# Performance work log

Measured on AMD Instinct MI355X. Metric: run time of the kernel, lower is better.

## Reference

```python
import jax, jax.numpy as jnp
import numpy as np

N, E, B, IN = 20000, 320000, 64, 192


def setup_inputs() -> dict:
    key = jax.random.key(0)
    ks = iter(jax.random.split(key, 80))
    d = {}
    d["x"] = jax.random.normal(next(ks), (N, IN), jnp.float32)
    d["edge_index"] = jax.random.randint(next(ks), (2, E), 0, N - 1)  # +1 shift stays < N
    d["edge_attr"] = jax.random.normal(next(ks), (E,), jnp.float32)
    d["batch"] = jnp.sort(jax.random.randint(next(ks), (N,), 0, B))

    def lin(i, o):
        w = jax.random.normal(next(ks), (i, o), jnp.float32) * (1.0 / i ** 0.5)
        return w, jnp.zeros((o,), jnp.float32)

    dims = [(IN, 4, 64), (256, 4, 64), (256, 6, 32)]  # (in_ch, heads, out_ch) per conv
    for l, (ic, h, c) in enumerate(dims, 1):
        hc = h * c
        d[f"Wq{l}"], d[f"bq{l}"] = lin(ic, hc)
        d[f"Wk{l}"], d[f"bk{l}"] = lin(ic, hc)
        d[f"Wv{l}"], d[f"bv{l}"] = lin(ic, hc)
        d[f"We{l}"] = jax.random.normal(next(ks), (1, hc), jnp.float32)  # lin_edge, no bias
        d[f"Ws{l}"], d[f"bs{l}"] = lin(ic, hc)  # root/skip weight
    d["g1"] = jnp.ones((256,), jnp.float32); d["be1"] = jnp.zeros((256,), jnp.float32)
    d["g2"] = jnp.ones((256,), jnp.float32); d["be2"] = jnp.zeros((256,), jnp.float32)
    d["fc1_w"], d["fc1_b"] = lin(192, 32)
    d["fc2_w"], d["fc2_b"] = lin(32, 2)
    return d


def seg_softmax(s, seg, n):
    # per-destination-node softmax over edges, [E, H]
    m = jax.ops.segment_max(s, seg, num_segments=n)
    m = jnp.where(jnp.isfinite(m), m, 0.0)
    ex = jnp.exp(s - m[seg])
    den = jax.ops.segment_sum(ex, seg, num_segments=n)
    return ex / (den[seg] + 1e-16)


def tconv(x, src, dst, e, Wq, bq, Wk, bk, Wv, bv, We, Ws, bs, h, c):
    # PyG TransformerConv (concat=True, root_weight=True, beta=False, eval -> no dropout)
    n = x.shape[0]
    q = (x @ Wq + bq).reshape(n, h, c)
    k = (x @ Wk + bk).reshape(n, h, c)
    v = (x @ Wv + bv).reshape(n, h, c)
    ee = (e @ We).reshape(-1, h, c)           # [E, h, c] edge embedding
    kj = k[src] + ee                           # gather keys along edges
    scores = jnp.einsum('ehc,ehc->eh', q[dst], kj) * (1.0 / c ** 0.5)
    alpha = seg_softmax(scores, dst, n)        # [E, h]
    msg = (v[src] + ee) * alpha[..., None]
    out = jax.ops.segment_sum(msg, dst, num_segments=n).reshape(n, h * c)
    return out + x @ Ws + bs, alpha


def ln(x, g, b):
    mu = x.mean(-1, keepdims=True)
    var = x.var(-1, keepdims=True)
    return g * (x - mu) / jnp.sqrt(var + 1e-5) + b


def _forward(x, edge_index, edge_attr, batch, Wq1, bq1, Wk1, bk1, Wv1, bv1, We1, Ws1, bs1, Wq2, bq2, Wk2, bk2, Wv2, bv2, We2, Ws2, bs2, Wq3, bq3, Wk3, bk3, Wv3, bv3, We3, Ws3, bs3, g1, be1, g2, be2, fc1_w, fc1_b, fc2_w, fc2_b):
    ei = edge_index + 1                       # replicates `edge_index += 1` in source
    src, dst = ei[0], ei[1]
    e = edge_attr[:, None]                    # edge_dim = 1
    x1, a1 = tconv(x, src, dst, e, Wq1, bq1, Wk1, bk1, Wv1, bv1, We1, Ws1, bs1, 4, 64)
    x1 = jax.nn.relu(ln(x1, g1, be1))
    x2, a2 = tconv(x1, src, dst, e, Wq2, bq2, Wk2, bk2, Wv2, bv2, We2, Ws2, bs2, 4, 64)
    x2 = jax.nn.relu(ln(x2, g2, be2))
    x3, a3 = tconv(x2, src, dst, e, Wq3, bq3, Wk3, bk3, Wv3, bv3, We3, Ws3, bs3, 6, 32)
    x3 = jax.nn.relu(x3)                      # note: norm3 exists in __init__ but is never applied
    xr = x + x3
    cnt = jax.ops.segment_sum(jnp.ones((xr.shape[0],), xr.dtype), batch, num_segments=B)
    pooled = jax.ops.segment_sum(xr, batch, num_segments=B) / jnp.maximum(cnt, 1.0)[:, None]
    h = jax.nn.relu(pooled @ fc1_w + fc1_b)
    logits = h @ fc2_w + fc2_b
    return logits, a1, a2, a3


def reference(x, edge_index, edge_attr, batch, Wq1, bq1, Wk1, bk1, Wv1, bv1, We1, Ws1, bs1, Wq2, bq2, Wk2, bk2, Wv2, bv2, We2, Ws2, bs2, Wq3, bq3, Wk3, bk3, Wv3, bv3, We3, Ws3, bs3, g1, be1, g2, be2, fc1_w, fc1_b, fc2_w, fc2_b):
    return _forward(x, edge_index, edge_attr, batch, Wq1, bq1, Wk1, bk1, Wv1, bv1, We1, Ws1, bs1, Wq2, bq2, Wk2, bk2, Wv2, bv2, We2, Ws2, bs2, Wq3, bq3, Wk3, bk3, Wv3, bv3, We3, Ws3, bs3, g1, be1, g2, be2, fc1_w, fc1_b, fc2_w, fc2_b)
```

## Files before the change

kernel.cpp:

```cpp
#include <hip/hip_runtime.h>
#include <cstdint>
#include <cstddef>

#define DEVINL __device__ __forceinline__

typedef short s16x8 __attribute__((ext_vector_type(8)));
typedef float f32x4 __attribute__((ext_vector_type(4)));
typedef unsigned short u16x4 __attribute__((ext_vector_type(4)));
typedef unsigned short u16x8 __attribute__((ext_vector_type(8)));

DEVINL unsigned short f2bf(float f) {
  unsigned u = __float_as_uint(f);
  unsigned r = (u + 0x7FFFu + ((u >> 16) & 1u)) >> 16;
  return (unsigned short)r;
}
DEVINL float bf2f(unsigned short b) { return __uint_as_float(((unsigned)b) << 16); }

__global__ __launch_bounds__(256) void fill_i32(int* __restrict__ p, int val, int n) {
  int i = blockIdx.x * 256 + threadIdx.x;
  if (i < n) p[i] = val;
}


__global__ __launch_bounds__(256) void cvt_split(const float* __restrict__ in,
                                                 unsigned short* __restrict__ hi,
                                                 unsigned short* __restrict__ lo, int n) {
  int i = blockIdx.x * 256 + threadIdx.x;
  if (i >= n) return;
  float f = in[i];
  unsigned short h = f2bf(f);
  float r = f - bf2f(h);
  hi[i] = h;
  lo[i] = f2bf(r);
}

struct CvtWArgs {
  const float* W[12];
  int K[12];
  int M[12];
};
__global__ __launch_bounds__(256) void cvt_w_all(CvtWArgs a,
                                                 unsigned short* __restrict__ Wh,
                                                 unsigned short* __restrict__ Wl) {
  int tid = blockIdx.x * 256 + threadIdx.x;
  int mat = tid >> 16;
  int off = tid & 65535;
  if (mat >= 12) return;
  int K = a.K[mat], M = a.M[mat];
  if (off >= K * M) return;
  int k = off / M, m = off - k * M;
  float f = a.W[mat][off];
  unsigned short h = f2bf(f);
  float r = f - bf2f(h);
  size_t dst = (size_t)mat * 65536 + (size_t)m * K + k;
  Wh[dst] = h;
  Wl[dst] = f2bf(r);
}

struct GemmArgs {
  const unsigned short* Wh[4];
  const unsigned short* Wl[4];
  const float* bias[4];
  float* out[4];
  int obf[4];
};

template <int KTOT>
__global__ __launch_bounds__(256, 3) void gemm4_lds(
    const unsigned short* __restrict__ Ah, const unsigned short* __restrict__ Al,
    GemmArgs args, int N, int M) {
  const int BK = 64;
  __shared__ unsigned short ash[128 * 64];
  __shared__ unsigned short asl[128 * 64];
  __shared__ unsigned short wsh[64 * 64];
  __shared__ unsigned short wsl[64 * 64];
  int tid = threadIdx.x;
  int wave = tid >> 6, lane = tid & 63;
  int lrow = lane & 15, quad = lane >> 4;
  int mt = M >> 6;
  int ntile = mt * 4;
  int id = blockIdx.x, nwg = gridDim.x;
  int q8 = nwg >> 3, r8 = nwg & 7;
  int xcd = id & 7, j8 = id >> 3;
  int wg = (xcd < r8 ? xcd * (q8 + 1) : r8 * (q8 + 1) + (xcd - r8) * q8) + j8;
  int by = wg / ntile;
  int bxx = wg - by * ntile;
  int z = bxx / mt;
  int colTile = bxx - z * mt;
  int row0 = by * 128;
  int col0 = colTile * 64;
  const unsigned short* __restrict__ Wh = args.Wh[z];
  const unsigned short* __restrict__ Wl = args.Wl[z];
  const bool full = (args.obf[z] == 0);

  int ar[4], asq[4];
  size_t agoff[4];
#pragma unroll
  for (int i = 0; i < 4; i++) {
    int c = tid + i * 256;
    ar[i] = c >> 3;
    int kq = c & 7;
    asq[i] = kq ^ (ar[i] & 7);
    int gr = row0 + ar[i]; if (gr >= N) gr = N - 1;
    agoff[i] = (size_t)gr * KTOT + kq * 8;
  }
  int wr[2], wsq[2];
  size_t wgoff[2];
#pragma unroll
  for (int i = 0; i < 2; i++) {
    int c = tid + i * 256;
    wr[i] = c >> 3;
    int kq = c & 7;
    wsq[i] = kq ^ (wr[i] & 7);
    wgoff[i] = (size_t)(col0 + wr[i]) * KTOT + kq * 8;
  }

  s16x8 pa_h[4], pa_l[4], pw_h[2], pw_l[2];
#pragma unroll
  for (int i = 0; i < 4; i++) {
    pa_h[i] = *(const s16x8*)(Ah + agoff[i]);
    pa_l[i] = *(const s16x8*)(Al + agoff[i]);
  }
#pragma unroll
  for (int i = 0; i < 2; i++) {
    pw_h[i] = *(const s16x8*)(Wh + wgoff[i]);
    if (full) pw_l[i] = *(const s16x8*)(Wl + wgoff[i]);
  }

  f32x4 acc[2][4] = {};

  for (int k0 = 0; k0 < KTOT; k0 += BK) {
    __syncthreads();
#pragma unroll
    for (int i = 0; i < 4; i++) {
      *(s16x8*)(ash + ar[i] * 64 + asq[i] * 8) = pa_h[i];
      *(s16x8*)(asl + ar[i] * 64 + asq[i] * 8) = pa_l[i];
    }
#pragma unroll
    for (int i = 0; i < 2; i++) {
      *(s16x8*)(wsh + wr[i] * 64 + wsq[i] * 8) = pw_h[i];
      if (full) *(s16x8*)(wsl + wr[i] * 64 + wsq[i] * 8) = pw_l[i];
    }
    if (k0 + BK < KTOT) {
      int kn = k0 + BK;
#pragma unroll
      for (int i = 0; i < 4; i++) {
        pa_h[i] = *(const s16x8*)(Ah + agoff[i] + kn);
        pa_l[i] = *(const s16x8*)(Al + agoff[i] + kn);
      }
#pragma unroll
      for (int i = 0; i < 2; i++) {
        pw_h[i] = *(const s16x8*)(Wh + wgoff[i] + kn);
        if (full) pw_l[i] = *(const s16x8*)(Wl + wgoff[i] + kn);
      }
    }
    __syncthreads();
#pragma unroll
    for (int kk = 0; kk < 2; kk++) {
      s16x8 fah[2], fal[2], fbh[4], fbl[4];
#pragma unroll
      for (int rf = 0; rf < 2; rf++) {
        int r = wave * 32 + rf * 16 + lrow;
        int sq = (kk * 4 + quad) ^ (lrow & 7);
        fah[rf] = *(const s16x8*)(ash + r * 64 + sq * 8);
        fal[rf] = *(const s16x8*)(asl + r * 64 + sq * 8);
      }
#pragma unroll
      for (int cf = 0; cf < 4; cf++) {
        int cc = cf * 16 + lrow;
        int sq = (kk * 4 + quad) ^ (lrow & 7);
        fbh[cf] = *(const s16x8*)(wsh + cc * 64 + sq * 8);
        if (full) fbl[cf] = *(const s16x8*)(wsl + cc * 64 + sq * 8);
      }
#pragma unroll
      for (int rf = 0; rf < 2; rf++)
#pragma unroll
        for (int cf = 0; cf < 4; cf++) {
          acc[rf][cf] = __builtin_amdgcn_mfma_f32_16x16x32_bf16(fah[rf], fbh[cf], acc[rf][cf], 0, 0, 0);
          acc[rf][cf] = __builtin_amdgcn_mfma_f32_16x16x32_bf16(fal[rf], fbh[cf], acc[rf][cf], 0, 0, 0);
          if (full)
            acc[rf][cf] = __builtin_amdgcn_mfma_f32_16x16x32_bf16(fah[rf], fbl[cf], acc[rf][cf], 0, 0, 0);
        }
    }
  }
  const float* __restrict__ bias = args.bias[z];
  int obf = args.obf[z];
  if (obf == 0) {
    float* __restrict__ C = args.out[z];
#pragma unroll
    for (int cf = 0; cf < 4; cf++) {
      int col = col0 + cf * 16 + lrow;
      float bv = bias[col];
#pragma unroll
      for (int rf = 0; rf < 2; rf++) {
        int rb = row0 + wave * 32 + rf * 16 + quad * 4;
#pragma unroll
        for (int r = 0; r < 4; r++) {
          int rr = rb + r;
          if (rr < N) C[(size_t)rr * M + col] = acc[rf][cf][r] + bv;
        }
      }
    }
  } else {
    __syncthreads();
#pragma unroll
    for (int cf = 0; cf < 4; cf++) {
      int col = cf * 16 + lrow;
      float bv = bias[col0 + col];
#pragma unroll
      for (int rf = 0; rf < 2; rf++) {
        int rl = wave * 32 + rf * 16 + quad * 4;
#pragma unroll
        for (int r = 0; r < 4; r++)
          ash[(rl + r) * 64 + col] = f2bf(acc[rf][cf][r] + bv);
      }
    }
    __syncthreads();
    unsigned short* __restrict__ C = (unsigned short*)args.out[z];
#pragma unroll
    for (int i = 0; i < 4; i++) {
      int c = tid + i * 256;
      int row = c >> 3, g8 = c & 7;
      int rr = row0 + row;
      if (rr < N)
        *(u16x8*)(C + (size_t)rr * M + col0 + g8 * 8) =
            *(const u16x8*)(ash + row * 64 + g8 * 8);
    }
  }
}


__global__ __launch_bounds__(256) void hist_dst(const int* __restrict__ dst,
                                                int* __restrict__ cnt, int E) {
  int e = blockIdx.x * 256 + threadIdx.x;
  if (e < E) atomicAdd(&cnt[dst[e] + 1], 1);
}

__global__ __launch_bounds__(1024) void scan_hist(const int* __restrict__ cnt,
                                                  int* __restrict__ start,
                                                  int* __restrict__ off, int N) {
  __shared__ int sums[1024];
  const int CH = 20;
  int t = threadIdx.x;
  int base = t * CH;
  int local[CH];
  int tot = 0;
  if (base < N) {
#pragma unroll
    for (int i = 0; i < CH; i++) { local[i] = cnt[base + i]; tot += local[i]; }
  }
  sums[t] = tot;
  __syncthreads();
  for (int d = 1; d < 1024; d <<= 1) {
    int v = (t >= d) ? sums[t - d] : 0;
    __syncthreads();
    sums[t] += v;
    __syncthreads();
  }
  if (base < N) {
    int run = (t == 0) ? 0 : sums[t - 1];
#pragma unroll
    for (int i = 0; i < CH; i++) { start[base + i] = run; off[base + i] = run; run += local[i]; }
    if (base + CH == N) start[N] = run;
  }
}

__global__ __launch_bounds__(256) void scatter_edges(
    const int* __restrict__ src, const int* __restrict__ dst,
    const float* __restrict__ ea, int* __restrict__ off,
    int2* __restrict__ se, int* __restrict__ eid_s, int E) {
  int e = blockIdx.x * 256 + threadIdx.x;
  if (e >= E) return;
  int d = dst[e] + 1;
  int pos = atomicAdd(&off[d], 1);
  se[pos] = make_int2(src[e] + 1, __float_as_int(ea[e]));
  eid_s[pos] = e;
}

template <int H, int ACT, int MODE>
__global__ __launch_bounds__(256) void attn_fused(
    const unsigned short* __restrict__ q, const unsigned short* __restrict__ kb,
    const unsigned short* __restrict__ vb, const float* __restrict__ We,
    const int* __restrict__ start, const int2* __restrict__ se,
    const int* __restrict__ eid_s,
    float* __restrict__ sc, float* __restrict__ outp,
    float* __restrict__ alpha, int Nn, float scale,
    const float* __restrict__ gam, const float* __restrict__ bet,
    unsigned short* __restrict__ hi, unsigned short* __restrict__ lo) {
  const int HC = ACT * 8;
  const int LPH2 = ACT / H;
  int w = (blockIdx.x * 256 + threadIdx.x) >> 6;
  int lane = threadIdx.x & 63;
  if (w >= Nn) return;
  int b = start[w], e = start[w + 1];
  int hlane = lane & 31, half = lane >> 5;
  bool act = hlane < ACT;
  int idx = hlane * 8;
  int head = hlane / LPH2;
  float q8[8], We8[8];
#pragma unroll
  for (int j = 0; j < 8; j++) { q8[j] = 0.f; We8[j] = 0.f; }
  if (act) {
    u16x8 qv = *(const u16x8*)(q + (size_t)w * HC + idx);
#pragma unroll
    for (int j = 0; j < 8; j++) q8[j] = bf2f(qv[j]);
    float4 w0 = *(const float4*)(We + idx);
    float4 w1 = *(const float4*)(We + idx + 4);
    We8[0] = w0.x; We8[1] = w0.y; We8[2] = w0.z; We8[3] = w0.w;
    We8[4] = w1.x; We8[5] = w1.y; We8[6] = w1.z; We8[7] = w1.w;
  }
  float qwe = 0.f;
#pragma unroll
  for (int j = 0; j < 8; j++) qwe = fmaf(q8[j], We8[j], qwe);
#pragma unroll
  for (int mm = 1; mm < LPH2; mm <<= 1) qwe += __shfl_xor(qwe, mm, 64);

  float l = 0.f, tv = 0.f;
  float accv[8] = {0.f, 0.f, 0.f, 0.f, 0.f, 0.f, 0.f, 0.f};

  auto step = [&](u16x8 kc, u16x8 vc, float eav, int pairpos) {
    bool vld = (pairpos + half) < e;
    float p = 0.f;
#pragma unroll
    for (int j = 0; j < 8; j++) p = fmaf(q8[j], bf2f(kc[j]), p);
#pragma unroll
    for (int mm = 1; mm < LPH2; mm <<= 1) p += __shfl_xor(p, mm, 64);
    float es = __expf((p + eav * qwe) * scale);
    if (!vld) es = 0.f;
    if (act && vld && (hlane % LPH2) == 0)
      sc[(size_t)(pairpos + half) * H + head] = es;
    l += es;
    tv = fmaf(es, eav, tv);
#pragma unroll
    for (int j = 0; j < 8; j++) accv[j] = fmaf(es, bf2f(vc[j]), accv[j]);
  };

  u16x8 z8 = {0, 0, 0, 0, 0, 0, 0, 0};
  u16x8 kS[4] = {z8, z8, z8, z8};
  u16x8 vS[4] = {z8, z8, z8, z8};
  float eaS[4] = {0.f, 0.f, 0.f, 0.f};

  auto preload = [&](int pairpos, int st) {
    int pp = pairpos + half;
    int pc = pp < e ? pp : (e - 1);
    int2 pr = se[pc];
    int s = pr.x;
    eaS[st] = __int_as_float(pr.y);
    if (act) {
      kS[st] = *(const u16x8*)(kb + (size_t)s * HC + idx);
      vS[st] = *(const u16x8*)(vb + (size_t)s * HC + idx);
    }
  };

#pragma unroll
  for (int j = 0; j < 4; j++) if (b + 2 * j < e) preload(b + 2 * j, j);

  for (int pos = b; pos < e; pos += 8) {
#pragma unroll
    for (int j = 0; j < 4; j++) {
      int pp = pos + 2 * j;
      if (pp < e) {
        u16x8 kc = kS[j];
        u16x8 vc = vS[j];
        float ec = eaS[j];
        if (pp + 8 < e) preload(pp + 8, j);
        step(kc, vc, ec, pp);
      }
    }
  }

  l += __shfl_xor(l, 32, 64);
  tv += __shfl_xor(tv, 32, 64);
#pragma unroll
  for (int j = 0; j < 8; j++) accv[j] += __shfl_xor(accv[j], 32, 64);

  float invl = 1.0f / (l + 1e-16f);
  if (MODE == 1) {
    if (half == 0) {
      const float* orow = outp + (size_t)w * HC + idx;
      float4 o0 = *(const float4*)orow;
      float4 o1 = *(const float4*)(orow + 4);
      float y[8] = {o0.x, o0.y, o0.z, o0.w, o1.x, o1.y, o1.z, o1.w};
#pragma unroll
      for (int j = 0; j < 8; j++) y[j] += (accv[j] + tv * We8[j]) * invl;
      float s = 0.f, s2 = 0.f;
#pragma unroll
      for (int j = 0; j < 8; j++) { s += y[j]; s2 = fmaf(y[j], y[j], s2); }
#pragma unroll
      for (int mm = 1; mm < 32; mm <<= 1) {
        s += __shfl_xor(s, mm, 64);
        s2 += __shfl_xor(s2, mm, 64);
      }
      float mu = s * (1.0f / 256.0f);
      float var = s2 * (1.0f / 256.0f) - mu * mu;
      float rinv = rsqrtf(var + 1e-5f);
      float4 g0 = *(const float4*)(gam + idx);
      float4 g1v = *(const float4*)(gam + idx + 4);
      float4 b0 = *(const float4*)(bet + idx);
      float4 b1 = *(const float4*)(bet + idx + 4);
      float gg[8] = {g0.x, g0.y, g0.z, g0.w, g1v.x, g1v.y, g1v.z, g1v.w};
      float bb[8] = {b0.x, b0.y, b0.z, b0.w, b1.x, b1.y, b1.z, b1.w};
      u16x8 yh, yl;
#pragma unroll
      for (int j = 0; j < 8; j++) {
        float t = fmaxf(fmaf((y[j] - mu) * rinv, gg[j], bb[j]), 0.f);
        unsigned short hh = f2bf(t);
        yh[j] = hh;
        yl[j] = f2bf(t - bf2f(hh));
      }
      *(u16x8*)(hi + (size_t)w * HC + idx) = yh;
      *(u16x8*)(lo + (size_t)w * HC + idx) = yl;
    }
  } else {
    if (act && half == 0) {
      float* orow = outp + (size_t)w * HC + idx;
      float4 o0 = *(float4*)orow;
      float4 o1 = *(float4*)(orow + 4);
      o0.x += (accv[0] + tv * We8[0]) * invl;
      o0.y += (accv[1] + tv * We8[1]) * invl;
      o0.z += (accv[2] + tv * We8[2]) * invl;
      o0.w += (accv[3] + tv * We8[3]) * invl;
      o1.x += (accv[4] + tv * We8[4]) * invl;
      o1.y += (accv[5] + tv * We8[5]) * invl;
      o1.z += (accv[6] + tv * We8[6]) * invl;
      o1.w += (accv[7] + tv * We8[7]) * invl;
      *(float4*)orow = o0;
      *(float4*)(orow + 4) = o1;
    }
  }
  {
    int len = e - b;
    const int PCH = 64 / H;
    int p_of = lane / H;
    int h_of = lane - p_of * H;
    float myinv = __shfl(invl, h_of * LPH2, 64);
    __threadfence_block();
    for (int base = 0; base < len; base += PCH) {
      int po = base + p_of;
      if (p_of < PCH && po < len) {
        int pos = b + po;
        float es = sc[(size_t)pos * H + h_of];
        alpha[(size_t)eid_s[pos] * H + h_of] = es * myinv;
      }
    }
  }
}


__global__ __launch_bounds__(192) void resid_pool2(
    const float* __restrict__ x, const float* __restrict__ x3,
    const int* __restrict__ batch, float* __restrict__ pooled,
    float* __restrict__ cnt, int N, int R) {
  int col = threadIdx.x;
  int r0 = blockIdx.x * R;
  int r1 = min(r0 + R, N);
  if (r0 >= N) return;
  float acc = 0.f;
  int cur = batch[r0];
  int run = 0;
  for (int r = r0; r < r1; r++) {
    int b = batch[r];
    if (b != cur) {
      atomicAdd(&pooled[cur * 192 + col], acc);
      if (col == 0) atomicAdd(&cnt[cur], (float)run);
      acc = 0.f; run = 0; cur = b;
    }
    size_t i = (size_t)r * 192 + col;
    acc += x[i] + fmaxf(x3[i], 0.f);
    run++;
  }
  atomicAdd(&pooled[cur * 192 + col], acc);
  if (col == 0) atomicAdd(&cnt[cur], (float)run);
}

__global__ __launch_bounds__(64) void head_mlp(
    const float* __restrict__ pooled, const float* __restrict__ cnt,
    const float* __restrict__ fc1w, const float* __restrict__ fc1b,
    const float* __restrict__ fc2w, const float* __restrict__ fc2b,
    float* __restrict__ logits) {
  int b = blockIdx.x;
  int t = threadIdx.x;
  __shared__ float p[192];
  __shared__ float hbuf[32];
  float inv = 1.0f / fmaxf(cnt[b], 1.0f);
  for (int i = t; i < 192; i += 64) p[i] = pooled[b * 192 + i] * inv;
  __syncthreads();
  if (t < 32) {
    float acc = fc1b[t];
    for (int i = 0; i < 192; i++) acc = fmaf(p[i], fc1w[i * 32 + t], acc);
    hbuf[t] = fmaxf(acc, 0.f);
  }
  __syncthreads();
  if (t < 2) {
    float acc = fc2b[t];
    for (int j = 0; j < 32; j++) acc = fmaf(hbuf[j], fc2w[j * 2 + t], acc);
    logits[b * 2 + t] = acc;
  }
}

static inline int divup(int a, int b) { return (a + b - 1) / b; }

extern "C" void kernel_launch(void* const* d_in, const int* in_sizes, int n_in,
                              void* d_out, int out_size, void* d_ws, size_t ws_size,
                              hipStream_t stream) {
  const int N = 20000, E = 320000, B = 64;
  const float* x     = (const float*)d_in[0];
  const int*   ei    = (const int*)d_in[1];
  const float* eattr = (const float*)d_in[2];
  const int*   batch = (const int*)d_in[3];
  const int* srcp = ei;
  const int* dstp = ei + E;

  const float* Wq[3]; const float* bq[3]; const float* Wk[3]; const float* bk[3];
  const float* Wv[3]; const float* bv[3]; const float* We[3]; const float* Ws[3];
  const float* bs[3];
  for (int l = 0; l < 3; l++) {
    int base = 4 + l * 9;
    Wq[l] = (const float*)d_in[base + 0]; bq[l] = (const float*)d_in[base + 1];
    Wk[l] = (const float*)d_in[base + 2]; bk[l] = (const float*)d_in[base + 3];
    Wv[l] = (const float*)d_in[base + 4]; bv[l] = (const float*)d_in[base + 5];
    We[l] = (const float*)d_in[base + 6];
    Ws[l] = (const float*)d_in[base + 7]; bs[l] = (const float*)d_in[base + 8];
  }
  const float* g1  = (const float*)d_in[31]; const float* be1 = (const float*)d_in[32];
  const float* g2  = (const float*)d_in[33]; const float* be2 = (const float*)d_in[34];
  const float* fc1w = (const float*)d_in[35]; const float* fc1b = (const float*)d_in[36];
  const float* fc2w = (const float*)d_in[37]; const float* fc2b = (const float*)d_in[38];

  float* out = (float*)d_out;
  float* logits = out;
  float* a1 = out + 128;
  float* a2 = a1 + (size_t)E * 4;
  float* a3 = a2 + (size_t)E * 4;

  float* ws = (float*)d_ws;
  size_t o = 0;
  float* qb = ws + o; o += (size_t)N * 256;
  float* kvb = ws + o; o += (size_t)N * 256;
  float* xa = ws + o; o += (size_t)N * 256;
  float* xb = ws + o; o += (size_t)N * 256;
  float* sc = ws + o; o += (size_t)E * 6;
  int*   cntb  = (int*)(ws + o); o += N;
  int*   startb= (int*)(ws + o); o += N + 1;
  int*   offb  = (int*)(ws + o); o += N + 1;
  int2*  se    = (int2*)(ws + o); o += (size_t)E * 2;
  int*   eid_s = (int*)(ws + o); o += E;
  float* pooled = ws + o; o += (size_t)B * 192;
  float* cnt    = ws + o; o += B;
  unsigned short* Ah = (unsigned short*)(ws + o); o += (size_t)N * 128;
  unsigned short* Al = (unsigned short*)(ws + o); o += (size_t)N * 128;
  unsigned short* Wh12 = (unsigned short*)(ws + o); o += (size_t)12 * 32768;
  unsigned short* Wl12 = (unsigned short*)(ws + o); o += (size_t)12 * 32768;

  unsigned short* qh = (unsigned short*)qb;
  unsigned short* kh = (unsigned short*)kvb;
  unsigned short* vh = kh + (size_t)N * 256;

  dim3 blk(256);

  struct LayerCfg { int K, M; float scale; };
  LayerCfg cfg[3] = {
    {192, 256, 0.125f},
    {256, 256, 0.125f},
    {256, 192, 0.1767766952966369f},
  };
  CvtWArgs cwa;
  for (int l = 0; l < 3; l++) {
    cwa.W[l * 4 + 0] = Wq[l]; cwa.W[l * 4 + 1] = Wk[l];
    cwa.W[l * 4 + 2] = Wv[l]; cwa.W[l * 4 + 3] = Ws[l];
    for (int zz = 0; zz < 4; zz++) {
      cwa.K[l * 4 + zz] = cfg[l].K; cwa.M[l * 4 + zz] = cfg[l].M;
    }
  }
  cvt_w_all<<<12 * 65536 / 256, blk, 0, stream>>>(cwa, Wh12, Wl12);

  fill_i32<<<divup(N, 256), blk, 0, stream>>>(cntb, 0, N);
  hist_dst<<<divup(E, 256), blk, 0, stream>>>(dstp, cntb, E);
  scan_hist<<<1, dim3(1024), 0, stream>>>(cntb, startb, offb, N);
  scatter_edges<<<divup(E, 256), blk, 0, stream>>>(srcp, dstp, eattr, offb,
                                                  se, eid_s, E);

  float*       lay_out[3] = {xb, xb, xa};
  float*       alpha_out[3] = {a1, a2, a3};
  const float* gams[3] = {g1, g2, nullptr};
  const float* bets[3] = {be1, be2, nullptr};

  cvt_split<<<divup(N * 192, 256), blk, 0, stream>>>(x, Ah, Al, N * 192);

  int stripes = divup(N, 128);
  for (int l = 0; l < 3; l++) {
    int M = cfg[l].M;
    GemmArgs ga;
    float* outs[4] = {(float*)qh, (float*)kh, (float*)vh, lay_out[l]};
    const float* biases[4] = {bq[l], bk[l], bv[l], bs[l]};
    int obfs[4] = {1, 1, 1, 0};
    for (int z = 0; z < 4; z++) {
      ga.Wh[z] = Wh12 + (size_t)(l * 4 + z) * 65536;
      ga.Wl[z] = Wl12 + (size_t)(l * 4 + z) * 65536;
      ga.bias[z] = biases[z];
      ga.out[z] = outs[z];
      ga.obf[z] = obfs[z];
    }
    dim3 gg((M >> 6) * 4 * stripes);
    if (l == 0)      gemm4_lds<192><<<gg, blk, 0, stream>>>(Ah, Al, ga, N, M);
    else             gemm4_lds<256><<<gg, blk, 0, stream>>>(Ah, Al, ga, N, M);

    dim3 gat(divup(N * 64, 256));
    if (l < 2) {
      attn_fused<4, 32, 1><<<gat, blk, 0, stream>>>(
          qh, kh, vh, We[l], startb, se, eid_s, sc, lay_out[l],
          alpha_out[l], N, cfg[l].scale, gams[l], bets[l], Ah, Al);
    } else {
      attn_fused<6, 24, 0><<<gat, blk, 0, stream>>>(
          qh, kh, vh, We[l], startb, se, eid_s, sc, lay_out[l],
          alpha_out[l], N, cfg[l].scale, nullptr, nullptr, nullptr, nullptr);
    }
  }

  fill_i32<<<divup(B * 192 + B, 256), blk, 0, stream>>>((int*)pooled, 0, B * 192 + B);
  resid_pool2<<<divup(N, 32), dim3(192), 0, stream>>>(x, xa, batch, pooled, cnt, N, 32);
  head_mlp<<<B, dim3(64), 0, stream>>>(pooled, cnt, fc1w, fc1b, fc2w, fc2b, logits);
}
```

Baseline: 562.6 us.

## Load GEMM tiles directly into LDS with global_load_lds

```diff
diff --git a/kernel.cpp b/kernel.cpp
--- a/kernel.cpp
+++ b/kernel.cpp
@@ -15,6 +15,12 @@
   return (unsigned short)r;
 }
 DEVINL float bf2f(unsigned short b) { return __uint_as_float(((unsigned)b) << 16); }
+
+DEVINL void gl16(const unsigned short* g, unsigned short* l) {
+  __builtin_amdgcn_global_load_lds(
+      (const __attribute__((address_space(1))) unsigned int*)g,
+      (__attribute__((address_space(3))) unsigned int*)l, 16, 0, 0);
+}
 
 __global__ __launch_bounds__(256) void fill_i32(int* __restrict__ p, int val, int n) {
   int i = blockIdx.x * 256 + threadIdx.x;
@@ -93,39 +99,8 @@
   const unsigned short* __restrict__ Wl = args.Wl[z];
   const bool full = (args.obf[z] == 0);
 
-  int ar[4], asq[4];
-  size_t agoff[4];
-#pragma unroll
-  for (int i = 0; i < 4; i++) {
-    int c = tid + i * 256;
-    ar[i] = c >> 3;
-    int kq = c & 7;
-    asq[i] = kq ^ (ar[i] & 7);
-    int gr = row0 + ar[i]; if (gr >= N) gr = N - 1;
-    agoff[i] = (size_t)gr * KTOT + kq * 8;
-  }
-  int wr[2], wsq[2];
-  size_t wgoff[2];
-#pragma unroll
-  for (int i = 0; i < 2; i++) {
-    int c = tid + i * 256;
-    wr[i] = c >> 3;
-    int kq = c & 7;
-    wsq[i] = kq ^ (wr[i] & 7);
-    wgoff[i] = (size_t)(col0 + wr[i]) * KTOT + kq * 8;
-  }
-
-  s16x8 pa_h[4], pa_l[4], pw_h[2], pw_l[2];
-#pragma unroll
-  for (int i = 0; i < 4; i++) {
-    pa_h[i] = *(const s16x8*)(Ah + agoff[i]);
-    pa_l[i] = *(const s16x8*)(Al + agoff[i]);
-  }
-#pragma unroll
-  for (int i = 0; i < 2; i++) {
-    pw_h[i] = *(const s16x8*)(Wh + wgoff[i]);
-    if (full) pw_l[i] = *(const s16x8*)(Wl + wgoff[i]);
-  }
+  int lr8 = lane >> 3;
+  int kq = lane & 7;
 
   f32x4 acc[2][4] = {};
 
@@ -133,27 +108,22 @@
     __syncthreads();
 #pragma unroll
     for (int i = 0; i < 4; i++) {
-      *(s16x8*)(ash + ar[i] * 64 + asq[i] * 8) = pa_h[i];
-      *(s16x8*)(asl + ar[i] * 64 + asq[i] * 8) = pa_l[i];
+      int s = wave + i * 4;
+      int row = s * 8 + lr8;
+      int gr = row0 + row; if (gr >= N) gr = N - 1;
+      size_t gofs = (size_t)gr * KTOT + k0 + ((kq ^ (row & 7)) * 8);
+      gl16(Ah + gofs, ash + s * 512);
+      gl16(Al + gofs, asl + s * 512);
     }
 #pragma unroll
     for (int i = 0; i < 2; i++) {
-      *(s16x8*)(wsh + wr[i] * 64 + wsq[i] * 8) = pw_h[i];
-      if (full) *(s16x8*)(wsl + wr[i] * 64 + wsq[i] * 8) = pw_l[i];
-    }
-    if (k0 + BK < KTOT) {
-      int kn = k0 + BK;
-#pragma unroll
-      for (int i = 0; i < 4; i++) {
-        pa_h[i] = *(const s16x8*)(Ah + agoff[i] + kn);
-        pa_l[i] = *(const s16x8*)(Al + agoff[i] + kn);
-      }
-#pragma unroll
-      for (int i = 0; i < 2; i++) {
-        pw_h[i] = *(const s16x8*)(Wh + wgoff[i] + kn);
-        if (full) pw_l[i] = *(const s16x8*)(Wl + wgoff[i] + kn);
-      }
-    }
+      int s = wave + i * 4;
+      int row = s * 8 + lr8;
+      size_t gofs = (size_t)(col0 + row) * KTOT + k0 + ((kq ^ (row & 7)) * 8);
+      gl16(Wh + gofs, wsh + s * 512);
+      if (full) gl16(Wl + gofs, wsl + s * 512);
+    }
+    asm volatile("s_waitcnt vmcnt(0)" ::: "memory");
     __syncthreads();
 #pragma unroll
     for (int kk = 0; kk < 2; kk++) {
```

New measurement: 533.9 us. -5.1%, faster.
